# Optimization experiments

Hardware: AMD Instinct MI355X
Metric: run time of the kernel (lower is better)

The kernel has to match this reference:

```python
import jax, jax.numpy as jnp
import numpy as np

N = 16384; C = 16; H = 256; W = 704
HEADS = 4; PTS = 4; K = 8; DH = C // HEADS
EPS = 1e-3  # BatchNorm eps from module

def _bn(x, g, b):
    # BatchNorm1d in training mode: batch statistics over N
    mu = x.mean(axis=0)
    var = x.var(axis=0)
    return (x - mu) * jax.lax.rsqrt(var + EPS) * g + b

def setup_inputs():
    key = jax.random.key(0)
    ks = jax.random.split(key, 20)
    def w(i, shape, s=0.25):
        return jax.random.normal(ks[i], shape, jnp.float32) * s
    grid_y = jax.random.randint(ks[0], (N,), 0, H)
    grid_x = jax.random.randint(ks[1], (N,), 0, W)
    return {
        "point_features": jax.random.normal(ks[2], (N, C), jnp.float32),
        "image_feat": jax.random.normal(ks[3], (C, H, W), jnp.float32),
        "image_grid": jnp.stack([grid_y, grid_x], axis=1),
        "Wk": w(4, (C, C)), "bk": w(5, (C,)), "gk": jnp.ones((C,)), "betak": jnp.zeros((C,)),
        "Wfc": w(6, (2, C)), "bfc": w(7, (C,)), "gfc": jnp.ones((C,)), "betafc": jnp.zeros((C,)),
        "Wt": w(8, (C, C)), "bt": w(9, (C,)), "gt": jnp.ones((C,)), "betat": jnp.zeros((C,)),
        "Woff": w(10, (C, HEADS * PTS * 2), 0.02), "boff": w(11, (HEADS * PTS * 2,), 0.5),
        "Wattn": w(12, (C, HEADS * PTS), 0.02), "battn": jnp.zeros((HEADS * PTS,)),
        "Wval": w(13, (C, C)), "bval": w(14, (C,)),
        "Wout": w(15, (C, C)), "bout": w(16, (C,)),
        "Wf": w(17, (2 * C, C)), "bf": w(18, (C,)), "gf": jnp.ones((C,)), "betaf": jnp.zeros((C,)),
    }

def _deform_attn(q, image_feat, grid_f, Woff, boff, Wattn, battn, Wval, bval, Wout, bout):
    # MSDeformAttn with 1 level: learned offsets around projected pixel, bilinear sampling
    n = q.shape[0]
    off = (q @ Woff + boff).reshape(n, HEADS, PTS, 2)
    attn = jax.nn.softmax((q @ Wattn + battn).reshape(n, HEADS, PTS), axis=-1)
    val = (image_feat.reshape(C, H * W).T @ Wval + bval).reshape(H * W, HEADS, DH)
    val_h = val.transpose(1, 0, 2)  # [HEADS, HW, DH]
    loc_y = grid_f[:, 0][:, None, None] + off[..., 0]  # [N, HEADS, PTS]
    loc_x = grid_f[:, 1][:, None, None] + off[..., 1]
    y0 = jnp.floor(loc_y); x0 = jnp.floor(loc_x)
    wy = loc_y - y0; wx = loc_x - x0

    def corner(yi, xi, wgt):
        valid = (yi >= 0) & (yi <= H - 1) & (xi >= 0) & (xi <= W - 1)
        yc = jnp.clip(yi, 0, H - 1).astype(jnp.int32)
        xc = jnp.clip(xi, 0, W - 1).astype(jnp.int32)
        idx = (yc * W + xc).transpose(1, 0, 2)  # [HEADS, N, PTS]
        g = jax.vmap(lambda v, i: v[i])(val_h, idx)  # [HEADS, N, PTS, DH]
        return g * (wgt * valid).transpose(1, 0, 2)[..., None]

    samp = (corner(y0, x0, (1 - wy) * (1 - wx))
            + corner(y0, x0 + 1, (1 - wy) * wx)
            + corner(y0 + 1, x0, wy * (1 - wx))
            + corner(y0 + 1, x0 + 1, wy * wx))  # [HEADS, N, PTS, DH]
    out = (samp * attn.transpose(1, 0, 2)[..., None]).sum(axis=2)  # [HEADS, N, DH]
    out = out.transpose(1, 0, 2).reshape(n, C)
    return out @ Wout + bout

def reference(point_features, image_feat, image_grid, Wk, bk, gk, betak, Wfc, bfc, gfc, betafc, Wt, bt, gt, betat, Woff, boff, Wattn, battn, Wval, bval, Wout, bout, Wf, bf, gf, betaf):
    grid_f = image_grid.astype(jnp.float32)
    # KNN over projected pixel coords (cKDTree.query k=K+1, drop self)
    d2 = ((grid_f[:, None, :] - grid_f[None, :, :]) ** 2).sum(-1)
    _, nidx = jax.lax.top_k(-d2, K + 1)
    nidx = nidx[:, 1:]  # [N, K]

    pts = _bn(point_features @ Wk + bk, gk, betak)  # pts_key_proj
    # normalized relative image-plane positions -> fc
    center = grid_f.mean(axis=0)
    rel = grid_f - center
    mx = jnp.abs(rel).max(axis=0)
    mx = jnp.where(mx == 0, 1.0, mx)
    pos = _bn((rel / mx) @ Wfc + bfc, gfc, betafc)

    # gather image feats at projected pixels + KNN-graph neighbor aggregation
    gathered = image_feat[:, image_grid[:, 0], image_grid[:, 1]].T  # [N, C]
    neigh = gathered[nidx].mean(axis=1)  # [N, C]

    q = pts + pos
    img_pre = _deform_attn(q, image_feat, grid_f, Woff, boff, Wattn, battn, Wval, bval, Wout, bout) + neigh

    pts_pre = _bn(pts @ Wt + bt, gt, betat)  # pts_transform
    fuse = jax.nn.relu(jnp.concatenate([pts_pre, img_pre], axis=-1))  # activate_out
    return jax.nn.relu(_bn(fuse @ Wf + bf, gf, betaf))  # fuse_conv
```

## Files before the change

### kernel.cpp

```cpp
#include <hip/hip_runtime.h>
#include <climits>

#define N_ 16384
#define C_ 16
#define H_ 256
#define W_ 704
#define HW_ (H_*W_)
#define NC_ (N_*C_)
#define EPS_ 1e-3f
#define HDR_ 512

typedef unsigned long long ull;


#define VAL_   (HDR_ + 9*NC_)
#define KNNI_  (VAL_ + HW_*16)
#define PARTF_ (KNNI_ + 378256)
#define PK_    (PARTF_ + 8192)
#define PFC_   (PARTF_ + 16384)
#define PT_    (PARTF_ + 24576)

#define CAP_ 6144

__device__ __forceinline__ float wsum64(float v){
#pragma unroll
  for (int o = 32; o > 0; o >>= 1) v += __shfl_down(v, o);
  return v;
}

#define LOAD16(dst, src) { const float4* _s=(const float4*)(src); float4 _a=_s[0],_b=_s[1],_c=_s[2],_d=_s[3]; \
  dst[0]=_a.x;dst[1]=_a.y;dst[2]=_a.z;dst[3]=_a.w; dst[4]=_b.x;dst[5]=_b.y;dst[6]=_b.z;dst[7]=_b.w; \
  dst[8]=_c.x;dst[9]=_c.y;dst[10]=_c.z;dst[11]=_c.w; dst[12]=_d.x;dst[13]=_d.y;dst[14]=_d.z;dst[15]=_d.w; }

#define STORE16(dst, src) { float4* _d=(float4*)(dst); \
  _d[0]=make_float4(src[0],src[1],src[2],src[3]); _d[1]=make_float4(src[4],src[5],src[6],src[7]); \
  _d[2]=make_float4(src[8],src[9],src[10],src[11]); _d[3]=make_float4(src[12],src[13],src[14],src[15]); }

__global__ __launch_bounds__(256) void k_init(float* ws){
  if (blockIdx.x < 176){
    int4* c = (int4*)(ws + KNNI_);
    c[blockIdx.x*256 + threadIdx.x] = make_int4(0,0,0,0);
  } else if (threadIdx.x == 0){
    int* ih = (int*)ws;
    ih[0]=0; ih[1]=0; ih[2]=INT_MAX; ih[3]=INT_MIN; ih[4]=INT_MAX; ih[5]=INT_MIN;
  }
}

__global__ __launch_bounds__(256) void k_gridcnt(const int* __restrict__ grid, float* __restrict__ ws){
  int i = blockIdx.x*256 + threadIdx.x;
  int2 p = ((const int2*)grid)[i];
  int* counts = (int*)(ws + KNNI_);
  atomicAdd(&counts[p.x*W_ + p.y], 1);
  int sy=p.x, sx=p.y, mny=p.x, mxy=p.x, mnx=p.y, mxx=p.y;
#pragma unroll
  for (int o=32;o>0;o>>=1){
    sy += __shfl_down(sy,o); sx += __shfl_down(sx,o);
    mny = min(mny,__shfl_down(mny,o)); mxy = max(mxy,__shfl_down(mxy,o));
    mnx = min(mnx,__shfl_down(mnx,o)); mxx = max(mxx,__shfl_down(mxx,o));
  }
  __shared__ int sh[24];
  int w = threadIdx.x >> 6;
  if ((threadIdx.x & 63) == 0){
    sh[w]=sy; sh[4+w]=sx; sh[8+w]=mny; sh[12+w]=mxy; sh[16+w]=mnx; sh[20+w]=mxx;
  }
  __syncthreads();
  if (threadIdx.x == 0){
    int a0=sh[0]+sh[1]+sh[2]+sh[3];
    int a1=sh[4]+sh[5]+sh[6]+sh[7];
    int a2=min(min(sh[8],sh[9]),min(sh[10],sh[11]));
    int a3=max(max(sh[12],sh[13]),max(sh[14],sh[15]));
    int a4=min(min(sh[16],sh[17]),min(sh[18],sh[19]));
    int a5=max(max(sh[20],sh[21]),max(sh[22],sh[23]));
    int* ih = (int*)ws;
    atomicAdd(&ih[0],a0); atomicAdd(&ih[1],a1);
    atomicMin(&ih[2],a2); atomicMax(&ih[3],a3);
    atomicMin(&ih[4],a4); atomicMax(&ih[5],a5);
  }
}

__global__ __launch_bounds__(256) void k_scanA(float* ws){
  const int* counts = (const int*)(ws + KNNI_);
  int* bsum = (int*)(ws + KNNI_) + 180224 + 180240;
  int t = threadIdx.x;
  int v = counts[blockIdx.x*256 + t];
#pragma unroll
  for (int o=32;o>0;o>>=1) v += __shfl_down(v,o);
  __shared__ int w4[4];
  if ((t&63)==0) w4[t>>6] = v;
  __syncthreads();
  if (t==0) bsum[blockIdx.x] = w4[0]+w4[1]+w4[2]+w4[3];
}

__global__ __launch_bounds__(256) void k_scanB(float* ws){
  if (threadIdx.x == 0){
    int* ih = (int*)ws;
    float cy = (float)ih[0] / (float)N_;
    float cx = (float)ih[1] / (float)N_;
    float my = fmaxf((float)ih[3]-cy, cy-(float)ih[2]);
    float mx = fmaxf((float)ih[5]-cx, cx-(float)ih[4]);
    if (my == 0.f) my = 1.f;
    if (mx == 0.f) mx = 1.f;
    ws[264]=cy; ws[265]=cx; ws[266]=1.f/my; ws[267]=1.f/mx;
  }
  int* bsum = (int*)(ws + KNNI_) + 180224 + 180240;
  int* boff = bsum + 704;
  __shared__ int sWsum[4];
  __shared__ int sCarry;
  int t = threadIdx.x, lane = t & 63, wv = t >> 6;
  if (t==0) sCarry = 0;
  __syncthreads();
  for (int c=0;c<3;++c){
    int idx = c*256 + t;
    int v0 = (idx < 704) ? bsum[idx] : 0;
    int v = v0;
#pragma unroll
    for (int o=1;o<64;o<<=1){ int xx=__shfl_up(v,o); if (lane>=o) v+=xx; }
    if (lane==63) sWsum[wv]=v;
    __syncthreads();
    int add = sCarry;
    for (int w2=0;w2<wv;++w2) add += sWsum[w2];
    if (idx < 704) boff[idx] = add + v - v0;
    __syncthreads();
    if (t==255) sCarry = add + v;
    __syncthreads();
  }
}

__global__ __launch_bounds__(256) void k_scanC(float* ws){
  int* counts = (int*)(ws + KNNI_);
  int* cellst = counts + 180224;
  const int* boff = counts + 180224 + 180240 + 704;
  __shared__ int sWsum[4];
  int t = threadIdx.x, lane = t & 63, wv = t >> 6;
  int i = blockIdx.x*256 + t;
  int v0 = counts[i], v = v0;
#pragma unroll
  for (int o=1;o<64;o<<=1){ int xx=__shfl_up(v,o); if (lane>=o) v+=xx; }
  if (lane==63) sWsum[wv]=v;
  __syncthreads();
  int add = boff[blockIdx.x];
  for (int w2=0;w2<wv;++w2) add += sWsum[w2];
  int start = add + v - v0;
  cellst[i] = start;
  counts[i] = start;
  if (i == 0) cellst[HW_] = N_;
}

__global__ __launch_bounds__(256) void k_scatter(const int* __restrict__ grid, float* __restrict__ ws){
  int i = blockIdx.x*256 + threadIdx.x;
  int2 g = ((const int2*)grid)[i];
  int* counts = (int*)(ws + KNNI_);
  unsigned* psort = (unsigned*)(counts + 180224 + 180240 + 704 + 704);
  int pos = atomicAdd(&counts[g.x*W_ + g.y], 1);
  psort[pos] = ((unsigned)g.x<<24) | ((unsigned)g.y<<14) | (unsigned)i;
}

__global__ __launch_bounds__(256) void k_prep(const float* __restrict__ imf,
                                              const int* __restrict__ grid,
                                              const float* __restrict__ Wval,
                                              const float* __restrict__ bval,
                                              float* __restrict__ ws){
  int t = threadIdx.x;
  if (blockIdx.x < 1024){
    int idx = blockIdx.x*256 + t;
    int i = idx >> 4, c = idx & 15;
    int2 g = ((const int2*)grid)[i];
    ws[HDR_ + 2*NC_ + idx] = imf[c*HW_ + g.x*W_ + g.y];
  } else {
    __shared__ float sW[256], sb[16];
    sW[t] = Wval[t];
    if (t < 16) sb[t] = bval[t];
    __syncthreads();
    int pix = (blockIdx.x-1024)*256 + t;
    float a[16];
#pragma unroll
    for (int ci=0;ci<16;++ci) a[ci] = imf[ci*HW_ + pix];
    float o[16];
#pragma unroll
    for (int c=0;c<16;++c) o[c] = sb[c];
#pragma unroll
    for (int ci=0;ci<16;++ci){ float v=a[ci];
#pragma unroll
      for (int c=0;c<16;++c) o[c] += v*sW[ci*16+c];
    }
    float* val = ws + VAL_;
    STORE16(val + pix*16, o);
  }
}

__device__ __forceinline__ void knn_insert(ull* arr, ull key){
  if (key < arr[8]){
    int q = 8;
    while (q > 0 && arr[q-1] > key){ arr[q] = arr[q-1]; --q; }
    arr[q] = key;
  }
}

__device__ __forceinline__ void scan_rows_global(const int* __restrict__ cellst,
                                                 const unsigned* __restrict__ psort,
                                                 int y, int x, int s,
                                                 int y0, int y1, int x0, int x1, ull* arr){
  for (int yy=y0+s; yy<=y1; yy+=4){
    int rowb = yy*W_;
    int st = cellst[rowb + x0];
    int e  = cellst[rowb + x1 + 1];
    int dy = y-yy, dy2 = dy*dy;
    for (int p=st; p<e; ++p){
      unsigned u = psort[p];
      int px = (int)((u>>14)&1023);
      int dx = x-px;
      knn_insert(arr, ((ull)(unsigned)(dy2+dx*dx) << 14) | (ull)(u & 16383u));
    }
  }
}

__device__ __forceinline__ void scan_rows_band(const unsigned* sBand, const int* sRowBase,
                                               int ya, int y, int x, int s,
                                               int y0, int y1, int x0, int x1, ull* arr){
  for (int yy=y0+s; yy<=y1; yy+=4){
    int j = yy-ya;
    int b = sRowBase[j], e = sRowBase[j+1];
    int lo=b, hi=e;
    while (lo<hi){ int mid=(lo+hi)>>1; int xm=(int)((sBand[mid]>>14)&1023); if (xm<x0) lo=mid+1; else hi=mid; }
    int dy = y-yy, dy2 = dy*dy;
    for (int p=lo; p<e; ++p){
      unsigned u = sBand[p];
      int px = (int)((u>>14)&1023);
      if (px > x1) break;
      int dx = x-px;
      knn_insert(arr, ((ull)(unsigned)(dy2+dx*dx) << 14) | (ull)(u & 16383u));
    }
  }
}

__global__ __launch_bounds__(256) void k_knn4(float* __restrict__ ws){
  const int* cellst = (const int*)(ws + KNNI_) + 180224;
  const unsigned* psort = (const unsigned*)((const int*)(ws + KNNI_) + 180224 + 180240 + 704 + 704);
  __shared__ unsigned sBand[CAP_];
  __shared__ int sRowBase[80];
  __shared__ int sMn, sMx;
  int tid = threadIdx.x, lane = tid & 63;
  int s = tid & 3, pl = tid >> 2;
  int gid = blockIdx.x*64 + pl;
  unsigned me = psort[gid];
  int y = (int)(me>>24), x = (int)((me>>14)&1023), i = (int)(me&16383);
  if (tid==0){ sMn = INT_MAX; sMx = -1; }
  __syncthreads();
  if (s==0){ atomicMin(&sMn, y); atomicMax(&sMx, y); }
  __syncthreads();
  int ya = max(sMn-16,0), yb = min(sMx+16,H_-1);
  int nr = yb-ya+1;
  int p0 = cellst[ya*W_], p1 = cellst[(yb+1)*W_];
  int count = p1-p0;
  bool fb = (count > CAP_) || (nr > 78);
  if (!fb){
    for (int j=tid; j<count; j+=256) sBand[j] = psort[p0+j];
    for (int j=tid; j<=nr; j+=256) sRowBase[j] = cellst[(ya+j)*W_] - p0;
  }
  __syncthreads();
  int r = 8;
  { int y0=max(y-8,0),y1=min(y+8,H_-1),x0=max(x-8,0),x1=min(x+8,W_-1);
    if ((y1-y0+1)*(x1-x0+1) < 224) r = 16; }
  ull arr[9];
#pragma unroll
  for (int q=0;q<9;++q) arr[q] = ~0ull;
  {
    int y0=max(y-r,0),y1=min(y+r,H_-1),x0=max(x-r,0),x1=min(x+r,W_-1);
    if (!fb) scan_rows_band(sBand, sRowBase, ya, y, x, s, y0, y1, x0, x1, arr);
    else     scan_rows_global(cellst, psort, y, x, s, y0, y1, x0, x1, arr);
  }
  ull m[9];
  bool done = false;
  {
    ull k[9];
#pragma unroll
    for (int q=0;q<9;++q) m[q] = ~0ull;
    int base = lane & ~3;
    for (int ss=0; ss<4; ++ss){
#pragma unroll
      for (int q=0;q<9;++q) k[q] = __shfl(arr[q], base+ss);
      for (int q2=0;q2<9;++q2){
        ull kk = k[q2];
        if (kk >= m[8]) break;
        int q = 8; while (q>0 && m[q-1]>kk){ m[q]=m[q-1]; --q; } m[q]=kk;
      }
    }
    int y0=max(y-r,0),y1=min(y+r,H_-1),x0=max(x-r,0),x1=min(x+r,W_-1);
    bool covered = (y0==0)&&(y1==H_-1)&&(x0==0)&&(x1==W_-1);
    bool ok = covered;
    if (!ok && m[8] != ~0ull){ int d9 = (int)(m[8]>>14); ok = d9 < (r+1)*(r+1); }
    done = ok;
  }
  while (__ballot(!done)){
    if (!done){
      r <<= 1;
      int y0=max(y-r,0),y1=min(y+r,H_-1),x0=max(x-r,0),x1=min(x+r,W_-1);
#pragma unroll
      for (int q=0;q<9;++q) arr[q] = ~0ull;
      if (!fb && r <= 16) scan_rows_band(sBand, sRowBase, ya, y, x, s, y0, y1, x0, x1, arr);
      else                scan_rows_global(cellst, psort, y, x, s, y0, y1, x0, x1, arr);
    }
    ull k[9];
    bool doIns = !done;
    if (doIns){
#pragma unroll
      for (int q=0;q<9;++q) m[q] = ~0ull;
    }
    int base = lane & ~3;
    for (int ss=0; ss<4; ++ss){
#pragma unroll
      for (int q=0;q<9;++q) k[q] = __shfl(arr[q], base+ss);
      if (doIns){
        for (int q2=0;q2<9;++q2){
          ull kk = k[q2];
          if (kk >= m[8]) break;
          int q = 8; while (q>0 && m[q-1]>kk){ m[q]=m[q-1]; --q; } m[q]=kk;
        }
      }
    }
    if (!done){
      int y0=max(y-r,0),y1=min(y+r,H_-1),x0=max(x-r,0),x1=min(x+r,W_-1);
      bool covered = (y0==0)&&(y1==H_-1)&&(x0==0)&&(x1==W_-1);
      bool ok = covered;
      if (!ok && m[8] != ~0ull){ int d9 = (int)(m[8]>>14); ok = d9 < (r+1)*(r+1); }
      if (ok) done = true;
    }
  }
  const float* gath = ws + HDR_ + 2*NC_;
  float4 acc = make_float4(0.f,0.f,0.f,0.f);
#pragma unroll
  for (int nb=1; nb<9; ++nb){
    int idx = (int)(m[nb] & 16383ull);
    const float4 g = *(const float4*)(gath + idx*16 + s*4);
    acc.x += g.x; acc.y += g.y; acc.z += g.z; acc.w += g.w;
  }
  float* neigh = ws + HDR_ + 7*NC_;
  *(float4*)(neigh + i*16 + s*4) =
      make_float4(acc.x*0.125f, acc.y*0.125f, acc.z*0.125f, acc.w*0.125f);
}

__global__ __launch_bounds__(64) void k_lin1(
    const float* __restrict__ pf, const int* __restrict__ grid,
    const float* __restrict__ Wk, const float* __restrict__ bk,
    const float* __restrict__ Wfc, const float* __restrict__ bfc,
    float* __restrict__ ws)
{
  __shared__ float sWk[256], sbk[16], sWfc[32], sbfc[16];
  int t = threadIdx.x;
  for (int j=t;j<256;j+=64) sWk[j] = Wk[j];
  if (t < 16){ sbk[t]=bk[t]; sbfc[t]=bfc[t]; }
  if (t < 32) sWfc[t] = Wfc[t];
  __syncthreads();
  int i = blockIdx.x*64 + t;
  float p[16]; LOAD16(p, pf + i*16);
  float ok[16];
#pragma unroll
  for (int c=0;c<16;++c) ok[c] = sbk[c];
#pragma unroll
  for (int j=0;j<16;++j){ float v = p[j];
#pragma unroll
    for (int c=0;c<16;++c) ok[c] += v*sWk[j*16+c];
  }
  float* pts_lin = ws + HDR_;
  STORE16(pts_lin + i*16, ok);
  float cy=ws[264], cx=ws[265], imy=ws[266], imx=ws[267];
  int2 g = ((const int2*)grid)[i];
  float ry = ((float)g.x - cy)*imy, rx = ((float)g.y - cx)*imx;
  float op[16];
#pragma unroll
  for (int c=0;c<16;++c) op[c] = ry*sWfc[c] + rx*sWfc[16+c] + sbfc[c];
  float* pos_lin = ws + HDR_ + NC_;
  STORE16(pos_lin + i*16, op);
  float* partK  = ws + PK_;
  float* partFC = ws + PFC_;
#pragma unroll
  for (int c=0;c<16;++c){
    float a = wsum64(ok[c]); float b = wsum64(ok[c]*ok[c]);
    if (t==0){ partK[blockIdx.x*32+c]=a; partK[blockIdx.x*32+16+c]=b; }
    a = wsum64(op[c]); b = wsum64(op[c]*op[c]);
    if (t==0){ partFC[blockIdx.x*32+c]=a; partFC[blockIdx.x*32+16+c]=b; }
  }
}

__device__ __forceinline__ void red1_body(const float* __restrict__ g, const float* __restrict__ b,
                                          float* __restrict__ ws, int partOff, int aOff, float* red){
  int t = threadIdx.x, slot = t & 31, chunk = t >> 5;
  const float* part = ws + partOff;
  float acc = 0.f;
  for (int bb=chunk*32; bb<chunk*32+32; ++bb) acc += part[bb*32 + slot];
  red[t] = acc;
  __syncthreads();
  if (chunk == 0){
    float v = red[slot];
#pragma unroll
    for (int k2=1;k2<8;++k2) v += red[k2*32+slot];
    red[slot] = v;
  }
  __syncthreads();
  if (t < 16){
    float mu  = red[t]    * (1.f/N_);
    float var = red[16+t] * (1.f/N_) - mu*mu;
    float a = g[t] / sqrtf(var + EPS_);
    ws[aOff+t]    = a;
    ws[aOff+16+t] = b[t] - mu*a;
  }
  __syncthreads();
}

__global__ __launch_bounds__(256) void k_red2(const float* __restrict__ gk, const float* __restrict__ betak,
                                              const float* __restrict__ gfc, const float* __restrict__ betafc,
                                              float* __restrict__ ws){
  __shared__ float red[256];
  red1_body(gk, betak, ws, PK_, 136, red);
  red1_body(gfc, betafc, ws, PFC_, 168, red);
}

__global__ __launch_bounds__(256) void k_red1(const float* __restrict__ g, const float* __restrict__ b,
                                              float* __restrict__ ws, int partOff, int aOff){
  __shared__ float red[256];
  red1_body(g, b, ws, partOff, aOff, red);
}

__global__ __launch_bounds__(64) void k_qstage(
    const float* __restrict__ Wt, const float* __restrict__ bt,
    const float* __restrict__ Woff, const float* __restrict__ boff,
    const float* __restrict__ Wattn, const float* __restrict__ battn,
    float* __restrict__ ws)
{
  __shared__ float sWt[256], sWoff[512], sWattn[256];
  __shared__ float sbt[16], sboff[32], sbattn[16];
  __shared__ float skA[16], skC[16], sfcA[16], sfcC[16];
  int t = threadIdx.x;
  for (int j=t;j<256;j+=64){ sWt[j]=Wt[j]; sWattn[j]=Wattn[j]; }
  for (int j=t;j<512;j+=64) sWoff[j]=Woff[j];
  if (t<16){ sbt[t]=bt[t]; sbattn[t]=battn[t];
    skA[t]=ws[136+t]; skC[t]=ws[152+t]; sfcA[t]=ws[168+t]; sfcC[t]=ws[184+t]; }
  if (t<32) sboff[t]=boff[t];
  __syncthreads();
  int i = blockIdx.x*64 + t;
  float* pts_lin = ws + HDR_;
  float* pos_lin = ws + HDR_ + NC_;
  float* t_lin   = ws + HDR_ + 3*NC_;
  float* offp    = ws + HDR_ + 4*NC_;
  float* attnp   = ws + HDR_ + 6*NC_;
  float pl[16], po[16];
  LOAD16(pl, pts_lin + i*16);
  LOAD16(po, pos_lin + i*16);
  float pts[16], q[16];
#pragma unroll
  for (int c=0;c<16;++c){ pts[c] = pl[c]*skA[c]+skC[c]; q[c] = pts[c] + po[c]*sfcA[c]+sfcC[c]; }
  float tv[16];
#pragma unroll
  for (int c=0;c<16;++c) tv[c] = sbt[c];
#pragma unroll
  for (int j=0;j<16;++j){ float v=pts[j];
#pragma unroll
    for (int c=0;c<16;++c) tv[c] += v*sWt[j*16+c];
  }
  STORE16(t_lin + i*16, tv);
  float* partT = ws + PT_;
#pragma unroll
  for (int c=0;c<16;++c){
    float a = wsum64(tv[c]); float b = wsum64(tv[c]*tv[c]);
    if (t==0){ partT[blockIdx.x*32+c]=a; partT[blockIdx.x*32+16+c]=b; }
  }
  float ov[32];
#pragma unroll
  for (int o=0;o<32;++o) ov[o] = sboff[o];
#pragma unroll
  for (int j=0;j<16;++j){ float v=q[j];
#pragma unroll
    for (int o=0;o<32;++o) ov[o] += v*sWoff[j*32+o];
  }
  { float4* d=(float4*)(offp + i*32);
#pragma unroll
    for (int r=0;r<8;++r) d[r]=make_float4(ov[r*4],ov[r*4+1],ov[r*4+2],ov[r*4+3]);
  }
  float l[16];
#pragma unroll
  for (int c=0;c<16;++c) l[c] = sbattn[c];
#pragma unroll
  for (int j=0;j<16;++j){ float v=q[j];
#pragma unroll
    for (int c=0;c<16;++c) l[c] += v*sWattn[j*16+c];
  }
  float av[16];
#pragma unroll
  for (int h=0;h<4;++h){
    float m = fmaxf(fmaxf(l[h*4],l[h*4+1]),fmaxf(l[h*4+2],l[h*4+3]));
    float e0=expf(l[h*4]-m), e1=expf(l[h*4+1]-m), e2=expf(l[h*4+2]-m), e3=expf(l[h*4+3]-m);
    float inv = 1.f/(e0+e1+e2+e3);
    av[h*4]=e0*inv; av[h*4+1]=e1*inv; av[h*4+2]=e2*inv; av[h*4+3]=e3*inv;
  }
  STORE16(attnp + i*16, av);
}

__global__ __launch_bounds__(256) void k_attn(
    const int* __restrict__ grid,
    const float* __restrict__ Wout, const float* __restrict__ bout,
    const float* __restrict__ Wf, const float* __restrict__ bf,
    float* __restrict__ ws)
{
  __shared__ float sWout[256], sWf[512], sbout[16], sbf[16];
  __shared__ float sTl[1024], sNei[1024], sSamp[1024], sImg[1024];
  __shared__ float sPart[128];
  int t = threadIdx.x;
  int p = t >> 2, h = t & 3;
  int i = blockIdx.x*64 + p;
  sWout[t]=Wout[t]; sWf[t]=Wf[t]; sWf[t+256]=Wf[t+256];
  if (t<16){ sbout[t]=bout[t]; sbf[t]=bf[t]; }
  {
    const float4* tl4 = (const float4*)(ws + HDR_ + 3*NC_ + blockIdx.x*1024);
    const float4* nv4 = (const float4*)(ws + HDR_ + 7*NC_ + blockIdx.x*1024);
    float4 v = tl4[t];
    int c0 = (t*4) & 15;
    float a0=ws[200+c0],a1=ws[200+c0+1],a2=ws[200+c0+2],a3=ws[200+c0+3];
    float c0v=ws[216+c0],c1v=ws[216+c0+1],c2v=ws[216+c0+2],c3v=ws[216+c0+3];
    sTl[t*4]   = fmaxf(v.x*a0+c0v, 0.f);
    sTl[t*4+1] = fmaxf(v.y*a1+c1v, 0.f);
    sTl[t*4+2] = fmaxf(v.z*a2+c2v, 0.f);
    sTl[t*4+3] = fmaxf(v.w*a3+c3v, 0.f);
    float4 nv = nv4[t];
    sNei[t*4]=nv.x; sNei[t*4+1]=nv.y; sNei[t*4+2]=nv.z; sNei[t*4+3]=nv.w;
  }
  const float4* off4 = (const float4*)(ws + HDR_ + 4*NC_ + blockIdx.x*2048);
  float4 o0 = off4[t*2], o1 = off4[t*2+1];
  float4 aw = ((const float4*)(ws + HDR_ + 6*NC_ + blockIdx.x*1024))[t];
  int2 g = ((const int2*)grid)[i];
  float y = (float)g.x, x = (float)g.y;
  const float4* val4 = (const float4*)(ws + VAL_);
  float4 acc = make_float4(0.f,0.f,0.f,0.f);
  float offv[8] = {o0.x,o0.y,o0.z,o0.w,o1.x,o1.y,o1.z,o1.w};
  float avv[4]  = {aw.x,aw.y,aw.z,aw.w};
#define CORNER(yy,xx,wgt) do{ int _y=(yy),_x=(xx); \
    if ((unsigned)_y < (unsigned)H_ && (unsigned)_x < (unsigned)W_){ \
      float4 _v = val4[(_y*W_+_x)*4 + h]; float _w = a*(wgt); \
      acc.x += _w*_v.x; acc.y += _w*_v.y; acc.z += _w*_v.z; acc.w += _w*_v.w; } }while(0)
#pragma unroll
  for (int pt=0; pt<4; ++pt){
    float a  = avv[pt];
    float ly = y + offv[pt*2], lx = x + offv[pt*2+1];
    float fy = floorf(ly), fx = floorf(lx);
    float wy = ly - fy, wx = lx - fx;
    int y0 = (int)fy, x0 = (int)fx;
    CORNER(y0,   x0,   (1.f-wy)*(1.f-wx));
    CORNER(y0,   x0+1, (1.f-wy)*wx);
    CORNER(y0+1, x0,   wy*(1.f-wx));
    CORNER(y0+1, x0+1, wy*wx);
  }
#undef CORNER
  ((float4*)sSamp)[t] = acc;
  __syncthreads();
  float img[4];
#pragma unroll
  for (int k=0;k<4;++k){ int cc=h*4+k; img[k] = sbout[cc] + sNei[p*16+cc]; }
#pragma unroll
  for (int j=0;j<16;++j){
    float v = sSamp[p*16+j];
#pragma unroll
    for (int k=0;k<4;++k) img[k] += v*sWout[j*16 + h*4 + k];
  }
  ((float4*)sImg)[t] = make_float4(img[0],img[1],img[2],img[3]);
  __syncthreads();
  float fl[4];
#pragma unroll
  for (int k=0;k<4;++k) fl[k] = sbf[h*4+k];
#pragma unroll
  for (int j=0;j<16;++j){
    float v1 = sTl[p*16+j];
    float v2 = fmaxf(sImg[p*16+j], 0.f);
#pragma unroll
    for (int k=0;k<4;++k){
      fl[k] += v1*sWf[j*16 + h*4 + k];
      fl[k] += v2*sWf[(16+j)*16 + h*4 + k];
    }
  }
  float* f_lin = ws + HDR_ + 8*NC_;
  ((float4*)(f_lin + blockIdx.x*1024))[t] = make_float4(fl[0],fl[1],fl[2],fl[3]);
  float s0=fl[0],s1=fl[1],s2=fl[2],s3=fl[3];
  float q0=fl[0]*fl[0],q1=fl[1]*fl[1],q2=fl[2]*fl[2],q3=fl[3]*fl[3];
#pragma unroll
  for (int o=32;o>=4;o>>=1){
    s0+=__shfl_down(s0,o); s1+=__shfl_down(s1,o); s2+=__shfl_down(s2,o); s3+=__shfl_down(s3,o);
    q0+=__shfl_down(q0,o); q1+=__shfl_down(q1,o); q2+=__shfl_down(q2,o); q3+=__shfl_down(q3,o);
  }
  int wave = t >> 6, lane = t & 63;
  if (lane < 4){
    sPart[wave*32 + lane*4+0]=s0; sPart[wave*32 + lane*4+1]=s1;
    sPart[wave*32 + lane*4+2]=s2; sPart[wave*32 + lane*4+3]=s3;
    sPart[wave*32 + 16 + lane*4+0]=q0; sPart[wave*32 + 16 + lane*4+1]=q1;
    sPart[wave*32 + 16 + lane*4+2]=q2; sPart[wave*32 + 16 + lane*4+3]=q3;
  }
  __syncthreads();
  if (t < 32){
    float v = sPart[t]+sPart[32+t]+sPart[64+t]+sPart[96+t];
    (ws + PARTF_)[blockIdx.x*32 + t] = v;
  }
}

__global__ __launch_bounds__(256) void k_out(const float* __restrict__ ws, float* __restrict__ out){
  int idx = blockIdx.x*256 + threadIdx.x;
  int c = idx & 15;
  float v = ws[HDR_ + 8*NC_ + idx];
  out[idx] = fmaxf(v*ws[232+c] + ws[248+c], 0.f);
}

extern "C" void kernel_launch(void* const* d_in, const int* in_sizes, int n_in,
                              void* d_out, int out_size, void* d_ws, size_t ws_size,
                              hipStream_t stream)
{
  const float* pf    = (const float*)d_in[0];
  const float* imf   = (const float*)d_in[1];
  const int*   gridp = (const int*)d_in[2];
  const float* Wk   =(const float*)d_in[3],  *bk   =(const float*)d_in[4];
  const float* gk   =(const float*)d_in[5],  *betak=(const float*)d_in[6];
  const float* Wfc  =(const float*)d_in[7],  *bfc  =(const float*)d_in[8];
  const float* gfc  =(const float*)d_in[9],  *betafc=(const float*)d_in[10];
  const float* Wt   =(const float*)d_in[11], *bt   =(const float*)d_in[12];
  const float* gt   =(const float*)d_in[13], *betat=(const float*)d_in[14];
  const float* Woff =(const float*)d_in[15], *boff =(const float*)d_in[16];
  const float* Wattn=(const float*)d_in[17], *battn=(const float*)d_in[18];
  const float* Wval =(const float*)d_in[19], *bval =(const float*)d_in[20];
  const float* Wout =(const float*)d_in[21], *bout =(const float*)d_in[22];
  const float* Wf   =(const float*)d_in[23], *bf   =(const float*)d_in[24];
  const float* gf   =(const float*)d_in[25], *betaf=(const float*)d_in[26];
  float* ws  = (float*)d_ws;
  float* out = (float*)d_out;

  hipLaunchKernelGGL(k_init,     dim3(177),      dim3(256), 0, stream, ws);
  hipLaunchKernelGGL(k_gridcnt,  dim3(N_/256),   dim3(256), 0, stream, gridp, ws);
  hipLaunchKernelGGL(k_scanA,    dim3(704),      dim3(256), 0, stream, ws);
  hipLaunchKernelGGL(k_scanB,    dim3(1),        dim3(256), 0, stream, ws);
  hipLaunchKernelGGL(k_scanC,    dim3(704),      dim3(256), 0, stream, ws);
  hipLaunchKernelGGL(k_scatter,  dim3(N_/256),   dim3(256), 0, stream, gridp, ws);
  hipLaunchKernelGGL(k_prep,     dim3(1728),     dim3(256), 0, stream, imf, gridp, Wval, bval, ws);
  hipLaunchKernelGGL(k_lin1,     dim3(N_/64),    dim3(64),  0, stream, pf, gridp, Wk, bk, Wfc, bfc, ws);
  hipLaunchKernelGGL(k_red2,     dim3(1),        dim3(256), 0, stream, gk, betak, gfc, betafc, ws);
  hipLaunchKernelGGL(k_qstage,   dim3(N_/64),    dim3(64),  0, stream, Wt, bt, Woff, boff, Wattn, battn, ws);
  hipLaunchKernelGGL(k_red1,     dim3(1),        dim3(256), 0, stream, gt, betat, ws, PT_, 200);
  hipLaunchKernelGGL(k_knn4,     dim3(N_/64),    dim3(256), 0, stream, ws);
  hipLaunchKernelGGL(k_attn,     dim3(N_/64),    dim3(256), 0, stream, gridp, Wout, bout, Wf, bf, ws);
  hipLaunchKernelGGL(k_red1,     dim3(1),        dim3(256), 0, stream, gf, betaf, ws, PARTF_, 232);
  hipLaunchKernelGGL(k_out,      dim3(NC_/256),  dim3(256), 0, stream, ws, out);
}
```

Baseline: 228.2 us.

## Compute BatchNorm stats analytically from input covariance and fuse stages into mega kernel

Computes the per-block second-moment matrix of the point features and grid moments in one pass, then derives the BatchNorm mean and variance for the key, position and transform layers in closed form. This removes the separate linear and reduction kernels, so the query, KNN, attention and fuse stages can run in one fused kernel, and the final BN and ReLU fold into a single output kernel. Launch count drops from fifteen to eight and intermediate round trips to memory are avoided. The trade-off is that variance computed as E[x²]−μ² in float can lose precision, and the single large kernel may have higher register pressure.

```diff
diff --git a/kernel.cpp b/kernel.cpp
--- a/kernel.cpp
+++ b/kernel.cpp
@@ -13,12 +13,13 @@
 typedef unsigned long long ull;
 
 
+#define GATH_  (HDR_ + 2*NC_)
+#define FLIN_  (HDR_ + 8*NC_)
 #define VAL_   (HDR_ + 9*NC_)
 #define KNNI_  (VAL_ + HW_*16)
 #define PARTF_ (KNNI_ + 378256)
-#define PK_    (PARTF_ + 8192)
-#define PFC_   (PARTF_ + 16384)
-#define PT_    (PARTF_ + 24576)
+#define PS_    (PARTF_ + 8192)
+#define GP_    (PS_ + 17408)
 
 #define CAP_ 6144
 
@@ -42,39 +43,88 @@
     c[blockIdx.x*256 + threadIdx.x] = make_int4(0,0,0,0);
   } else if (threadIdx.x == 0){
     int* ih = (int*)ws;
-    ih[0]=0; ih[1]=0; ih[2]=INT_MAX; ih[3]=INT_MIN; ih[4]=INT_MAX; ih[5]=INT_MIN;
-  }
-}
-
-__global__ __launch_bounds__(256) void k_gridcnt(const int* __restrict__ grid, float* __restrict__ ws){
-  int i = blockIdx.x*256 + threadIdx.x;
-  int2 p = ((const int2*)grid)[i];
-  int* counts = (int*)(ws + KNNI_);
-  atomicAdd(&counts[p.x*W_ + p.y], 1);
-  int sy=p.x, sx=p.y, mny=p.x, mxy=p.x, mnx=p.y, mxx=p.y;
-#pragma unroll
-  for (int o=32;o>0;o>>=1){
-    sy += __shfl_down(sy,o); sx += __shfl_down(sx,o);
-    mny = min(mny,__shfl_down(mny,o)); mxy = max(mxy,__shfl_down(mxy,o));
-    mnx = min(mnx,__shfl_down(mnx,o)); mxx = max(mxx,__shfl_down(mxx,o));
-  }
-  __shared__ int sh[24];
-  int w = threadIdx.x >> 6;
-  if ((threadIdx.x & 63) == 0){
-    sh[w]=sy; sh[4+w]=sx; sh[8+w]=mny; sh[12+w]=mxy; sh[16+w]=mnx; sh[20+w]=mxx;
-  }
-  __syncthreads();
-  if (threadIdx.x == 0){
-    int a0=sh[0]+sh[1]+sh[2]+sh[3];
-    int a1=sh[4]+sh[5]+sh[6]+sh[7];
-    int a2=min(min(sh[8],sh[9]),min(sh[10],sh[11]));
-    int a3=max(max(sh[12],sh[13]),max(sh[14],sh[15]));
-    int a4=min(min(sh[16],sh[17]),min(sh[18],sh[19]));
-    int a5=max(max(sh[20],sh[21]),max(sh[22],sh[23]));
-    int* ih = (int*)ws;
-    atomicAdd(&ih[0],a0); atomicAdd(&ih[1],a1);
-    atomicMin(&ih[2],a2); atomicMax(&ih[3],a3);
-    atomicMin(&ih[4],a4); atomicMax(&ih[5],a5);
+    ih[2]=INT_MAX; ih[3]=INT_MIN; ih[4]=INT_MAX; ih[5]=INT_MIN;
+  }
+}
+
+__global__ __launch_bounds__(256) void k_statsprep(
+    const float* __restrict__ pf, const float* __restrict__ imf,
+    const int* __restrict__ grid,
+    const float* __restrict__ Wval, const float* __restrict__ bval,
+    float* __restrict__ ws)
+{
+  int t = threadIdx.x;
+  if (blockIdx.x < 64){
+    __shared__ float sP[4096];
+    __shared__ double sDP[20];
+    __shared__ int sh[16];
+    int i = blockIdx.x*256 + t;
+    { const float4* s4=(const float4*)(pf+i*16);
+      float4* d4=(float4*)(sP+t*16);
+      d4[0]=s4[0]; d4[1]=s4[1]; d4[2]=s4[2]; d4[3]=s4[3]; }
+    int2 g = ((const int2*)grid)[i];
+    int* counts = (int*)(ws + KNNI_);
+    atomicAdd(&counts[g.x*W_ + g.y], 1);
+    int mny=g.x,mxy=g.x,mnx=g.y,mxx=g.y;
+#pragma unroll
+    for (int o=32;o>0;o>>=1){
+      mny=min(mny,__shfl_down(mny,o)); mxy=max(mxy,__shfl_down(mxy,o));
+      mnx=min(mnx,__shfl_down(mnx,o)); mxx=max(mxx,__shfl_down(mxx,o));
+    }
+    int wv = t>>6;
+    if ((t&63)==0){ sh[wv]=mny; sh[4+wv]=mxy; sh[8+wv]=mnx; sh[12+wv]=mxx; }
+    double yy=(double)g.x, xx=(double)g.y;
+    double m0=yy,m1=xx,m2=yy*yy,m3=xx*xx,m4=yy*xx;
+#pragma unroll
+    for (int o=32;o>0;o>>=1){
+      m0+=__shfl_down(m0,o); m1+=__shfl_down(m1,o); m2+=__shfl_down(m2,o);
+      m3+=__shfl_down(m3,o); m4+=__shfl_down(m4,o);
+    }
+    if ((t&63)==0){ sDP[wv*5]=m0; sDP[wv*5+1]=m1; sDP[wv*5+2]=m2; sDP[wv*5+3]=m3; sDP[wv*5+4]=m4; }
+    __syncthreads();
+    if (t==0){
+      int* ih=(int*)ws;
+      atomicMin(&ih[2],min(min(sh[0],sh[1]),min(sh[2],sh[3])));
+      atomicMax(&ih[3],max(max(sh[4],sh[5]),max(sh[6],sh[7])));
+      atomicMin(&ih[4],min(min(sh[8],sh[9]),min(sh[10],sh[11])));
+      atomicMax(&ih[5],max(max(sh[12],sh[13]),max(sh[14],sh[15])));
+      double* GP=(double*)(ws+GP_)+blockIdx.x*5;
+#pragma unroll
+      for (int k=0;k<5;++k) GP[k]=sDP[k]+sDP[5+k]+sDP[10+k]+sDP[15+k];
+    }
+    float* PS = ws + PS_ + blockIdx.x*272;
+    int a=t&15, b2=t>>4;
+    float acc=0.f;
+    for (int i2=0;i2<256;++i2) acc += sP[i2*16+a]*sP[i2*16+b2];
+    PS[16+t]=acc;
+    if (t<16){
+      float s=0.f;
+      for (int i2=0;i2<256;++i2) s += sP[i2*16+t];
+      PS[t]=s;
+    }
+  } else if (blockIdx.x < 1088){
+    int idx=(blockIdx.x-64)*256+t;
+    int i=idx>>4, c=idx&15;
+    int2 g=((const int2*)grid)[i];
+    ws[GATH_+idx]=imf[c*HW_+g.x*W_+g.y];
+  } else {
+    __shared__ float sW[256], sb[16];
+    sW[t]=Wval[t];
+    if (t<16) sb[t]=bval[t];
+    __syncthreads();
+    int pix=(blockIdx.x-1088)*256+t;
+    float a[16];
+#pragma unroll
+    for (int ci=0;ci<16;++ci) a[ci]=imf[ci*HW_+pix];
+    float o[16];
+#pragma unroll
+    for (int c=0;c<16;++c) o[c]=sb[c];
+#pragma unroll
+    for (int ci=0;ci<16;++ci){ float v=a[ci];
+#pragma unroll
+      for (int c=0;c<16;++c) o[c]+=v*sW[ci*16+c];
+    }
+    STORE16(ws+VAL_+pix*16, o);
   }
 }
 
@@ -91,37 +141,129 @@
   if (t==0) bsum[blockIdx.x] = w4[0]+w4[1]+w4[2]+w4[3];
 }
 
-__global__ __launch_bounds__(256) void k_scanB(float* ws){
-  if (threadIdx.x == 0){
-    int* ih = (int*)ws;
-    float cy = (float)ih[0] / (float)N_;
-    float cx = (float)ih[1] / (float)N_;
-    float my = fmaxf((float)ih[3]-cy, cy-(float)ih[2]);
-    float mx = fmaxf((float)ih[5]-cx, cx-(float)ih[4]);
-    if (my == 0.f) my = 1.f;
-    if (mx == 0.f) mx = 1.f;
-    ws[264]=cy; ws[265]=cx; ws[266]=1.f/my; ws[267]=1.f/mx;
-  }
+__global__ __launch_bounds__(256) void k_scanB(
+    const float* __restrict__ Wk, const float* __restrict__ bk,
+    const float* __restrict__ gk, const float* __restrict__ betak,
+    const float* __restrict__ Wfc, const float* __restrict__ bfc,
+    const float* __restrict__ gfc, const float* __restrict__ betafc,
+    const float* __restrict__ Wt, const float* __restrict__ bt,
+    const float* __restrict__ gt, const float* __restrict__ betat,
+    float* __restrict__ ws)
+{
+  __shared__ float sS[256], sSum[16];
+  __shared__ float skA[16], skC[16];
+  __shared__ double sG[5];
+  __shared__ float sCtr[4];
+  int t = threadIdx.x;
+  const float* PS = ws + PS_;
+  float acc=0.f, acc2=0.f;
+  for (int b=0;b<64;++b){
+    acc += PS[b*272 + t];
+    if (t<16) acc2 += PS[b*272 + 256 + t];
+  }
+  if (t<16){ sSum[t]=acc; sS[240+t]=acc2; }
+  else sS[t-16]=acc;
+  if (t<5){
+    const double* GP=(const double*)(ws+GP_);
+    double s=0.0;
+    for (int b=0;b<64;++b) s += GP[b*5+t];
+    sG[t]=s;
+  }
+  __syncthreads();
+  if (t==0){
+    const int* ih=(const int*)ws;
+    float cy=(float)(sG[0]/(double)N_), cx=(float)(sG[1]/(double)N_);
+    float my=fmaxf((float)ih[3]-cy, cy-(float)ih[2]);
+    float mx=fmaxf((float)ih[5]-cx, cx-(float)ih[4]);
+    if (my==0.f) my=1.f;
+    if (mx==0.f) mx=1.f;
+    sCtr[0]=cy; sCtr[1]=cx; sCtr[2]=1.f/my; sCtr[3]=1.f/mx;
+    ws[264]=cy; ws[265]=cx; ws[266]=sCtr[2]; ws[267]=sCtr[3];
+  }
+  __syncthreads();
+  const float invN = 1.f/(float)N_;
+  if (t<16){
+    float wc[16];
+#pragma unroll
+    for (int j=0;j<16;++j) wc[j]=Wk[j*16+t];
+    float dotS=0.f;
+#pragma unroll
+    for (int a2=0;a2<16;++a2) dotS+=sSum[a2]*wc[a2];
+    float qd=0.f;
+#pragma unroll
+    for (int b2=0;b2<16;++b2){
+      float inner=0.f;
+#pragma unroll
+      for (int a2=0;a2<16;++a2) inner+=wc[a2]*sS[b2*16+a2];
+      qd+=wc[b2]*inner;
+    }
+    float bkc=bk[t];
+    float mu = dotS*invN + bkc;
+    float ex2 = qd*invN + 2.f*bkc*dotS*invN + bkc*bkc;
+    float var = ex2 - mu*mu;
+    float a = gk[t]/sqrtf(var+EPS_);
+    skA[t]=a; skC[t]=betak[t]-mu*a;
+    ws[136+t]=a; ws[152+t]=skC[t];
+    float cy=sCtr[0], cx=sCtr[1], imy=sCtr[2], imx=sCtr[3];
+    float Eyy=((float)(sG[2]/(double)N_) - cy*cy)*imy*imy;
+    float Exx=((float)(sG[3]/(double)N_) - cx*cx)*imx*imx;
+    float Eyx=((float)(sG[4]/(double)N_) - cy*cx)*imy*imx;
+    float W0=Wfc[t], W1=Wfc[16+t];
+    float varfc = Eyy*W0*W0 + 2.f*Eyx*W0*W1 + Exx*W1*W1;
+    float afc = gfc[t]/sqrtf(varfc+EPS_);
+    ws[168+t]=afc; ws[184+t]=betafc[t]-bfc[t]*afc;
+  }
+  __syncthreads();
+  if (t<16){
+    float Ac[16];
+#pragma unroll
+    for (int j=0;j<16;++j){
+      float s=0.f;
+#pragma unroll
+      for (int m=0;m<16;++m) s += Wk[j*16+m]*skA[m]*Wt[m*16+t];
+      Ac[j]=s;
+    }
+    float dc=bt[t];
+#pragma unroll
+    for (int m=0;m<16;++m) dc += (bk[m]*skA[m]+skC[m])*Wt[m*16+t];
+    float dotS=0.f;
+#pragma unroll
+    for (int a2=0;a2<16;++a2) dotS+=sSum[a2]*Ac[a2];
+    float qd=0.f;
+#pragma unroll
+    for (int b2=0;b2<16;++b2){
+      float inner=0.f;
+#pragma unroll
+      for (int a2=0;a2<16;++a2) inner+=Ac[a2]*sS[b2*16+a2];
+      qd+=Ac[b2]*inner;
+    }
+    float mu = dotS*invN + dc;
+    float ex2 = qd*invN + 2.f*dc*dotS*invN + dc*dc;
+    float var = ex2 - mu*mu;
+    float a = gt[t]/sqrtf(var+EPS_);
+    ws[200+t]=a; ws[216+t]=betat[t]-mu*a;
+  }
+  __syncthreads();
   int* bsum = (int*)(ws + KNNI_) + 180224 + 180240;
   int* boff = bsum + 704;
   __shared__ int sWsum[4];
   __shared__ int sCarry;
-  int t = threadIdx.x, lane = t & 63, wv = t >> 6;
-  if (t==0) sCarry = 0;
+  int lane=t&63, wv=t>>6;
+  if (t==0) sCarry=0;
   __syncthreads();
   for (int c=0;c<3;++c){
-    int idx = c*256 + t;
-    int v0 = (idx < 704) ? bsum[idx] : 0;
-    int v = v0;
+    int idx=c*256+t;
+    int v0=(idx<704)?bsum[idx]:0;
+    int v=v0;
 #pragma unroll
     for (int o=1;o<64;o<<=1){ int xx=__shfl_up(v,o); if (lane>=o) v+=xx; }
     if (lane==63) sWsum[wv]=v;
     __syncthreads();
-    int add = sCarry;
-    for (int w2=0;w2<wv;++w2) add += sWsum[w2];
-    if (idx < 704) boff[idx] = add + v - v0;
-    __syncthreads();
-    if (t==255) sCarry = add + v;
+    int add=sCarry;
+    for (int w2=0;w2<wv;++w2) add+=sWsum[w2];
+    if (idx<704) boff[idx]=add+v-v0;
+    __syncthreads();
+    if (t==255) sCarry=add+v;
     __syncthreads();
   }
 }
@@ -131,68 +273,35 @@
   int* cellst = counts + 180224;
   const int* boff = counts + 180224 + 180240 + 704;
   __shared__ int sWsum[4];
-  int t = threadIdx.x, lane = t & 63, wv = t >> 6;
-  int i = blockIdx.x*256 + t;
-  int v0 = counts[i], v = v0;
+  int t=threadIdx.x, lane=t&63, wv=t>>6;
+  int i=blockIdx.x*256+t;
+  int v0=counts[i], v=v0;
 #pragma unroll
   for (int o=1;o<64;o<<=1){ int xx=__shfl_up(v,o); if (lane>=o) v+=xx; }
   if (lane==63) sWsum[wv]=v;
   __syncthreads();
-  int add = boff[blockIdx.x];
-  for (int w2=0;w2<wv;++w2) add += sWsum[w2];
-  int start = add + v - v0;
-  cellst[i] = start;
-  counts[i] = start;
-  if (i == 0) cellst[HW_] = N_;
+  int add=boff[blockIdx.x];
+  for (int w2=0;w2<wv;++w2) add+=sWsum[w2];
+  int start=add+v-v0;
+  cellst[i]=start;
+  counts[i]=start;
+  if (i==0) cellst[HW_]=N_;
 }
 
 __global__ __launch_bounds__(256) void k_scatter(const int* __restrict__ grid, float* __restrict__ ws){
-  int i = blockIdx.x*256 + threadIdx.x;
-  int2 g = ((const int2*)grid)[i];
-  int* counts = (int*)(ws + KNNI_);
-  unsigned* psort = (unsigned*)(counts + 180224 + 180240 + 704 + 704);
-  int pos = atomicAdd(&counts[g.x*W_ + g.y], 1);
-  psort[pos] = ((unsigned)g.x<<24) | ((unsigned)g.y<<14) | (unsigned)i;
-}
-
-__global__ __launch_bounds__(256) void k_prep(const float* __restrict__ imf,
-                                              const int* __restrict__ grid,
-                                              const float* __restrict__ Wval,
-                                              const float* __restrict__ bval,
-                                              float* __restrict__ ws){
-  int t = threadIdx.x;
-  if (blockIdx.x < 1024){
-    int idx = blockIdx.x*256 + t;
-    int i = idx >> 4, c = idx & 15;
-    int2 g = ((const int2*)grid)[i];
-    ws[HDR_ + 2*NC_ + idx] = imf[c*HW_ + g.x*W_ + g.y];
-  } else {
-    __shared__ float sW[256], sb[16];
-    sW[t] = Wval[t];
-    if (t < 16) sb[t] = bval[t];
-    __syncthreads();
-    int pix = (blockIdx.x-1024)*256 + t;
-    float a[16];
-#pragma unroll
-    for (int ci=0;ci<16;++ci) a[ci] = imf[ci*HW_ + pix];
-    float o[16];
-#pragma unroll
-    for (int c=0;c<16;++c) o[c] = sb[c];
-#pragma unroll
-    for (int ci=0;ci<16;++ci){ float v=a[ci];
-#pragma unroll
-      for (int c=0;c<16;++c) o[c] += v*sW[ci*16+c];
-    }
-    float* val = ws + VAL_;
-    STORE16(val + pix*16, o);
-  }
+  int i=blockIdx.x*256+threadIdx.x;
+  int2 g=((const int2*)grid)[i];
+  int* counts=(int*)(ws+KNNI_);
+  unsigned* psort=(unsigned*)(counts+180224+180240+704+704);
+  int pos=atomicAdd(&counts[g.x*W_+g.y],1);
+  psort[pos]=((unsigned)g.x<<24)|((unsigned)g.y<<14)|(unsigned)i;
 }
 
 __device__ __forceinline__ void knn_insert(ull* arr, ull key){
   if (key < arr[8]){
-    int q = 8;
-    while (q > 0 && arr[q-1] > key){ arr[q] = arr[q-1]; --q; }
-    arr[q] = key;
+    int q=8;
+    while (q>0 && arr[q-1]>key){ arr[q]=arr[q-1]; --q; }
+    arr[q]=key;
   }
 }
 
@@ -201,15 +310,15 @@
                                                  int y, int x, int s,
                                                  int y0, int y1, int x0, int x1, ull* arr){
   for (int yy=y0+s; yy<=y1; yy+=4){
-    int rowb = yy*W_;
-    int st = cellst[rowb + x0];
-    int e  = cellst[rowb + x1 + 1];
-    int dy = y-yy, dy2 = dy*dy;
-    for (int p=st; p<e; ++p){
-      unsigned u = psort[p];
-      int px = (int)((u>>14)&1023);
-      int dx = x-px;
-      knn_insert(arr, ((ull)(unsigned)(dy2+dx*dx) << 14) | (ull)(u & 16383u));
+    int rowb=yy*W_;
+    int st=cellst[rowb+x0];
+    int e =cellst[rowb+x1+1];
+    int dy=y-yy, dy2=dy*dy;
+    for (int p=st;p<e;++p){
+      unsigned u=psort[p];
+      int px=(int)((u>>14)&1023);
+      int dx=x-px;
+      knn_insert(arr, ((ull)(unsigned)(dy2+dx*dx)<<14)|(ull)(u&16383u));
     }
   }
 }
@@ -218,391 +327,331 @@
                                                int ya, int y, int x, int s,
                                                int y0, int y1, int x0, int x1, ull* arr){
   for (int yy=y0+s; yy<=y1; yy+=4){
-    int j = yy-ya;
-    int b = sRowBase[j], e = sRowBase[j+1];
+    int j=yy-ya;
+    int b=sRowBase[j], e=sRowBase[j+1];
     int lo=b, hi=e;
     while (lo<hi){ int mid=(lo+hi)>>1; int xm=(int)((sBand[mid]>>14)&1023); if (xm<x0) lo=mid+1; else hi=mid; }
-    int dy = y-yy, dy2 = dy*dy;
-    for (int p=lo; p<e; ++p){
-      unsigned u = sBand[p];
-      int px = (int)((u>>14)&1023);
-      if (px > x1) break;
-      int dx = x-px;
-      knn_insert(arr, ((ull)(unsigned)(dy2+dx*dx) << 14) | (ull)(u & 16383u));
-    }
-  }
-}
-
-__global__ __launch_bounds__(256) void k_knn4(float* __restrict__ ws){
-  const int* cellst = (const int*)(ws + KNNI_) + 180224;
-  const unsigned* psort = (const unsigned*)((const int*)(ws + KNNI_) + 180224 + 180240 + 704 + 704);
-  __shared__ unsigned sBand[CAP_];
-  __shared__ int sRowBase[80];
-  __shared__ int sMn, sMx;
-  int tid = threadIdx.x, lane = tid & 63;
-  int s = tid & 3, pl = tid >> 2;
-  int gid = blockIdx.x*64 + pl;
-  unsigned me = psort[gid];
-  int y = (int)(me>>24), x = (int)((me>>14)&1023), i = (int)(me&16383);
-  if (tid==0){ sMn = INT_MAX; sMx = -1; }
-  __syncthreads();
-  if (s==0){ atomicMin(&sMn, y); atomicMax(&sMx, y); }
-  __syncthreads();
-  int ya = max(sMn-16,0), yb = min(sMx+16,H_-1);
-  int nr = yb-ya+1;
-  int p0 = cellst[ya*W_], p1 = cellst[(yb+1)*W_];
-  int count = p1-p0;
-  bool fb = (count > CAP_) || (nr > 78);
-  if (!fb){
-    for (int j=tid; j<count; j+=256) sBand[j] = psort[p0+j];
-    for (int j=tid; j<=nr; j+=256) sRowBase[j] = cellst[(ya+j)*W_] - p0;
-  }
-  __syncthreads();
-  int r = 8;
-  { int y0=max(y-8,0),y1=min(y+8,H_-1),x0=max(x-8,0),x1=min(x+8,W_-1);
-    if ((y1-y0+1)*(x1-x0+1) < 224) r = 16; }
-  ull arr[9];
-#pragma unroll
-  for (int q=0;q<9;++q) arr[q] = ~0ull;
-  {
-    int y0=max(y-r,0),y1=min(y+r,H_-1),x0=max(x-r,0),x1=min(x+r,W_-1);
-    if (!fb) scan_rows_band(sBand, sRowBase, ya, y, x, s, y0, y1, x0, x1, arr);
-    else     scan_rows_global(cellst, psort, y, x, s, y0, y1, x0, x1, arr);
-  }
-  ull m[9];
-  bool done = false;
-  {
-    ull k[9];
-#pragma unroll
-    for (int q=0;q<9;++q) m[q] = ~0ull;
-    int base = lane & ~3;
-    for (int ss=0; ss<4; ++ss){
-#pragma unroll
-      for (int q=0;q<9;++q) k[q] = __shfl(arr[q], base+ss);
-      for (int q2=0;q2<9;++q2){
-        ull kk = k[q2];
-        if (kk >= m[8]) break;
-        int q = 8; while (q>0 && m[q-1]>kk){ m[q]=m[q-1]; --q; } m[q]=kk;
-      }
-    }
-    int y0=max(y-r,0),y1=min(y+r,H_-1),x0=max(x-r,0),x1=min(x+r,W_-1);
-    bool covered = (y0==0)&&(y1==H_-1)&&(x0==0)&&(x1==W_-1);
-    bool ok = covered;
-    if (!ok && m[8] != ~0ull){ int d9 = (int)(m[8]>>14); ok = d9 < (r+1)*(r+1); }
-    done = ok;
-  }
-  while (__ballot(!done)){
-    if (!done){
-      r <<= 1;
-      int y0=max(y-r,0),y1=min(y+r,H_-1),x0=max(x-r,0),x1=min(x+r,W_-1);
-#pragma unroll
-      for (int q=0;q<9;++q) arr[q] = ~0ull;
-      if (!fb && r <= 16) scan_rows_band(sBand, sRowBase, ya, y, x, s, y0, y1, x0, x1, arr);
-      else                scan_rows_global(cellst, psort, y, x, s, y0, y1, x0, x1, arr);
-    }
-    ull k[9];
-    bool doIns = !done;
-    if (doIns){
-#pragma unroll
-      for (int q=0;q<9;++q) m[q] = ~0ull;
-    }
-    int base = lane & ~3;
-    for (int ss=0; ss<4; ++ss){
-#pragma unroll
-      for (int q=0;q<9;++q) k[q] = __shfl(arr[q], base+ss);
-      if (doIns){
-        for (int q2=0;q2<9;++q2){
-          ull kk = k[q2];
-          if (kk >= m[8]) break;
-          int q = 8; while (q>0 && m[q-1]>kk){ m[q]=m[q-1]; --q; } m[q]=kk;
-        }
-      }
-    }
-    if (!done){
-      int y0=max(y-r,0),y1=min(y+r,H_-1),x0=max(x-r,0),x1=min(x+r,W_-1);
-      bool covered = (y0==0)&&(y1==H_-1)&&(x0==0)&&(x1==W_-1);
-      bool ok = covered;
-      if (!ok && m[8] != ~0ull){ int d9 = (int)(m[8]>>14); ok = d9 < (r+1)*(r+1); }
-      if (ok) done = true;
-    }
-  }
-  const float* gath = ws + HDR_ + 2*NC_;
-  float4 acc = make_float4(0.f,0.f,0.f,0.f);
-#pragma unroll
-  for (int nb=1; nb<9; ++nb){
-    int idx = (int)(m[nb] & 16383ull);
-    const float4 g = *(const float4*)(gath + idx*16 + s*4);
-    acc.x += g.x; acc.y += g.y; acc.z += g.z; acc.w += g.w;
-  }
-  float* neigh = ws + HDR_ + 7*NC_;
-  *(float4*)(neigh + i*16 + s*4) =
-      make_float4(acc.x*0.125f, acc.y*0.125f, acc.z*0.125f, acc.w*0.125f);
-}
-
-__global__ __launch_bounds__(64) void k_lin1(
-    const float* __restrict__ pf, const int* __restrict__ grid,
+    int dy=y-yy, dy2=dy*dy;
+    for (int p=lo;p<e;++p){
+      unsigned u=sBand[p];
+      int px=(int)((u>>14)&1023);
+      if (px>x1) break;
+      int dx=x-px;
+      knn_insert(arr, ((ull)(unsigned)(dy2+dx*dx)<<14)|(ull)(u&16383u));
+    }
+  }
+}
+
+__global__ __launch_bounds__(256) void k_mega(
+    const float* __restrict__ pf,
     const float* __restrict__ Wk, const float* __restrict__ bk,
     const float* __restrict__ Wfc, const float* __restrict__ bfc,
-    float* __restrict__ ws)
-{
-  __shared__ float sWk[256], sbk[16], sWfc[32], sbfc[16];
-  int t = threadIdx.x;
-  for (int j=t;j<256;j+=64) sWk[j] = Wk[j];
-  if (t < 16){ sbk[t]=bk[t]; sbfc[t]=bfc[t]; }
-  if (t < 32) sWfc[t] = Wfc[t];
-  __syncthreads();
-  int i = blockIdx.x*64 + t;
-  float p[16]; LOAD16(p, pf + i*16);
-  float ok[16];
-#pragma unroll
-  for (int c=0;c<16;++c) ok[c] = sbk[c];
-#pragma unroll
-  for (int j=0;j<16;++j){ float v = p[j];
-#pragma unroll
-    for (int c=0;c<16;++c) ok[c] += v*sWk[j*16+c];
-  }
-  float* pts_lin = ws + HDR_;
-  STORE16(pts_lin + i*16, ok);
-  float cy=ws[264], cx=ws[265], imy=ws[266], imx=ws[267];
-  int2 g = ((const int2*)grid)[i];
-  float ry = ((float)g.x - cy)*imy, rx = ((float)g.y - cx)*imx;
-  float op[16];
-#pragma unroll
-  for (int c=0;c<16;++c) op[c] = ry*sWfc[c] + rx*sWfc[16+c] + sbfc[c];
-  float* pos_lin = ws + HDR_ + NC_;
-  STORE16(pos_lin + i*16, op);
-  float* partK  = ws + PK_;
-  float* partFC = ws + PFC_;
-#pragma unroll
-  for (int c=0;c<16;++c){
-    float a = wsum64(ok[c]); float b = wsum64(ok[c]*ok[c]);
-    if (t==0){ partK[blockIdx.x*32+c]=a; partK[blockIdx.x*32+16+c]=b; }
-    a = wsum64(op[c]); b = wsum64(op[c]*op[c]);
-    if (t==0){ partFC[blockIdx.x*32+c]=a; partFC[blockIdx.x*32+16+c]=b; }
-  }
-}
-
-__device__ __forceinline__ void red1_body(const float* __restrict__ g, const float* __restrict__ b,
-                                          float* __restrict__ ws, int partOff, int aOff, float* red){
-  int t = threadIdx.x, slot = t & 31, chunk = t >> 5;
-  const float* part = ws + partOff;
-  float acc = 0.f;
-  for (int bb=chunk*32; bb<chunk*32+32; ++bb) acc += part[bb*32 + slot];
-  red[t] = acc;
-  __syncthreads();
-  if (chunk == 0){
-    float v = red[slot];
-#pragma unroll
-    for (int k2=1;k2<8;++k2) v += red[k2*32+slot];
-    red[slot] = v;
-  }
-  __syncthreads();
-  if (t < 16){
-    float mu  = red[t]    * (1.f/N_);
-    float var = red[16+t] * (1.f/N_) - mu*mu;
-    float a = g[t] / sqrtf(var + EPS_);
-    ws[aOff+t]    = a;
-    ws[aOff+16+t] = b[t] - mu*a;
-  }
-  __syncthreads();
-}
-
-__global__ __launch_bounds__(256) void k_red2(const float* __restrict__ gk, const float* __restrict__ betak,
-                                              const float* __restrict__ gfc, const float* __restrict__ betafc,
-                                              float* __restrict__ ws){
-  __shared__ float red[256];
-  red1_body(gk, betak, ws, PK_, 136, red);
-  red1_body(gfc, betafc, ws, PFC_, 168, red);
-}
-
-__global__ __launch_bounds__(256) void k_red1(const float* __restrict__ g, const float* __restrict__ b,
-                                              float* __restrict__ ws, int partOff, int aOff){
-  __shared__ float red[256];
-  red1_body(g, b, ws, partOff, aOff, red);
-}
-
-__global__ __launch_bounds__(64) void k_qstage(
     const float* __restrict__ Wt, const float* __restrict__ bt,
     const float* __restrict__ Woff, const float* __restrict__ boff,
     const float* __restrict__ Wattn, const float* __restrict__ battn,
-    float* __restrict__ ws)
-{
-  __shared__ float sWt[256], sWoff[512], sWattn[256];
-  __shared__ float sbt[16], sboff[32], sbattn[16];
-  __shared__ float skA[16], skC[16], sfcA[16], sfcC[16];
-  int t = threadIdx.x;
-  for (int j=t;j<256;j+=64){ sWt[j]=Wt[j]; sWattn[j]=Wattn[j]; }
-  for (int j=t;j<512;j+=64) sWoff[j]=Woff[j];
-  if (t<16){ sbt[t]=bt[t]; sbattn[t]=battn[t];
-    skA[t]=ws[136+t]; skC[t]=ws[152+t]; sfcA[t]=ws[168+t]; sfcC[t]=ws[184+t]; }
-  if (t<32) sboff[t]=boff[t];
-  __syncthreads();
-  int i = blockIdx.x*64 + t;
-  float* pts_lin = ws + HDR_;
-  float* pos_lin = ws + HDR_ + NC_;
-  float* t_lin   = ws + HDR_ + 3*NC_;
-  float* offp    = ws + HDR_ + 4*NC_;
-  float* attnp   = ws + HDR_ + 6*NC_;
-  float pl[16], po[16];
-  LOAD16(pl, pts_lin + i*16);
-  LOAD16(po, pos_lin + i*16);
-  float pts[16], q[16];
-#pragma unroll
-  for (int c=0;c<16;++c){ pts[c] = pl[c]*skA[c]+skC[c]; q[c] = pts[c] + po[c]*sfcA[c]+sfcC[c]; }
-  float tv[16];
-#pragma unroll
-  for (int c=0;c<16;++c) tv[c] = sbt[c];
-#pragma unroll
-  for (int j=0;j<16;++j){ float v=pts[j];
-#pragma unroll
-    for (int c=0;c<16;++c) tv[c] += v*sWt[j*16+c];
-  }
-  STORE16(t_lin + i*16, tv);
-  float* partT = ws + PT_;
-#pragma unroll
-  for (int c=0;c<16;++c){
-    float a = wsum64(tv[c]); float b = wsum64(tv[c]*tv[c]);
-    if (t==0){ partT[blockIdx.x*32+c]=a; partT[blockIdx.x*32+16+c]=b; }
-  }
-  float ov[32];
-#pragma unroll
-  for (int o=0;o<32;++o) ov[o] = sboff[o];
-#pragma unroll
-  for (int j=0;j<16;++j){ float v=q[j];
-#pragma unroll
-    for (int o=0;o<32;++o) ov[o] += v*sWoff[j*32+o];
-  }
-  { float4* d=(float4*)(offp + i*32);
-#pragma unroll
-    for (int r=0;r<8;++r) d[r]=make_float4(ov[r*4],ov[r*4+1],ov[r*4+2],ov[r*4+3]);
-  }
-  float l[16];
-#pragma unroll
-  for (int c=0;c<16;++c) l[c] = sbattn[c];
-#pragma unroll
-  for (int j=0;j<16;++j){ float v=q[j];
-#pragma unroll
-    for (int c=0;c<16;++c) l[c] += v*sWattn[j*16+c];
-  }
-  float av[16];
-#pragma unroll
-  for (int h=0;h<4;++h){
-    float m = fmaxf(fmaxf(l[h*4],l[h*4+1]),fmaxf(l[h*4+2],l[h*4+3]));
-    float e0=expf(l[h*4]-m), e1=expf(l[h*4+1]-m), e2=expf(l[h*4+2]-m), e3=expf(l[h*4+3]-m);
-    float inv = 1.f/(e0+e1+e2+e3);
-    av[h*4]=e0*inv; av[h*4+1]=e1*inv; av[h*4+2]=e2*inv; av[h*4+3]=e3*inv;
-  }
-  STORE16(attnp + i*16, av);
-}
-
-__global__ __launch_bounds__(256) void k_attn(
-    const int* __restrict__ grid,
     const float* __restrict__ Wout, const float* __restrict__ bout,
     const float* __restrict__ Wf, const float* __restrict__ bf,
     float* __restrict__ ws)
 {
-  __shared__ float sWout[256], sWf[512], sbout[16], sbf[16];
-  __shared__ float sTl[1024], sNei[1024], sSamp[1024], sImg[1024];
+  __shared__ float sWk[256], sWt[256], sWattn[256], sWout[256];
+  __shared__ float sWoff[512], sWf[512], sWfc[32];
+  __shared__ float sbk[16], sbfc[16], sbt[16], sboff[32], sbattn[16], sbout[16], sbf[16];
+  __shared__ float skA[16], skC[16], sfcA[16], sfcC[16], stA[16], stC[16];
+  __shared__ float sCtr[4];
+  __shared__ unsigned sMe[64];
+  __shared__ int sMn, sMx;
+  __shared__ unsigned sBand[CAP_];
+  __shared__ int sRowBase[80];
+  __shared__ float sTl[1024], sNei[1024], sOf[2048], sAt[1024], sSamp[1024], sImg[1024];
   __shared__ float sPart[128];
-  int t = threadIdx.x;
-  int p = t >> 2, h = t & 3;
-  int i = blockIdx.x*64 + p;
-  sWout[t]=Wout[t]; sWf[t]=Wf[t]; sWf[t+256]=Wf[t+256];
-  if (t<16){ sbout[t]=bout[t]; sbf[t]=bf[t]; }
+
+  const int* cellst = (const int*)(ws+KNNI_)+180224;
+  const unsigned* psort = (const unsigned*)((const int*)(ws+KNNI_)+180224+180240+704+704);
+  int tid=threadIdx.x, lane=tid&63;
+  sWk[tid]=Wk[tid]; sWt[tid]=Wt[tid]; sWattn[tid]=Wattn[tid]; sWout[tid]=Wout[tid];
+  sWoff[tid]=Woff[tid]; sWoff[256+tid]=Woff[256+tid];
+  sWf[tid]=Wf[tid]; sWf[256+tid]=Wf[256+tid];
+  if (tid<32){ sWfc[tid]=Wfc[tid]; sboff[tid]=boff[tid]; }
+  if (tid<16){
+    sbk[tid]=bk[tid]; sbfc[tid]=bfc[tid]; sbt[tid]=bt[tid]; sbattn[tid]=battn[tid];
+    sbout[tid]=bout[tid]; sbf[tid]=bf[tid];
+    skA[tid]=ws[136+tid]; skC[tid]=ws[152+tid];
+    sfcA[tid]=ws[168+tid]; sfcC[tid]=ws[184+tid];
+    stA[tid]=ws[200+tid]; stC[tid]=ws[216+tid];
+  }
+  if (tid<4) sCtr[tid]=ws[264+tid];
+  if (tid==0){ sMn=INT_MAX; sMx=-1; }
+  if (tid<64) sMe[tid]=psort[blockIdx.x*64+tid];
+  __syncthreads();
+  if (tid<64){
+    int yy=(int)(sMe[tid]>>24);
+    atomicMin(&sMn,yy); atomicMax(&sMx,yy);
+  }
+  __syncthreads();
+  int ya=max(sMn-16,0), yb=min(sMx+16,H_-1);
+  int nr=yb-ya+1;
+  int p0=cellst[ya*W_], p1=cellst[(yb+1)*W_];
+  int count=p1-p0;
+  bool fb=(count>CAP_)||(nr>78);
+  if (tid<64){
+    unsigned me=sMe[tid];
+    int i=(int)(me&16383u);
+    float yf=(float)(me>>24), xf=(float)((me>>14)&1023u);
+    float p[16]; LOAD16(p, pf+i*16);
+    float ok[16];
+#pragma unroll
+    for (int c=0;c<16;++c) ok[c]=sbk[c];
+#pragma unroll
+    for (int j=0;j<16;++j){ float v=p[j];
+#pragma unroll
+      for (int c=0;c<16;++c) ok[c]+=v*sWk[j*16+c];
+    }
+    float ry=(yf-sCtr[0])*sCtr[2], rx=(xf-sCtr[1])*sCtr[3];
+    float pts[16], q[16];
+#pragma unroll
+    for (int c=0;c<16;++c){
+      pts[c]=ok[c]*skA[c]+skC[c];
+      float pos=ry*sWfc[c]+rx*sWfc[16+c]+sbfc[c];
+      q[c]=pts[c]+pos*sfcA[c]+sfcC[c];
+    }
+    float tv[16];
+#pragma unroll
+    for (int c=0;c<16;++c) tv[c]=sbt[c];
+#pragma unroll
+    for (int j=0;j<16;++j){ float v=pts[j];
+#pragma unroll
+      for (int c=0;c<16;++c) tv[c]+=v*sWt[j*16+c];
+    }
+#pragma unroll
+    for (int c=0;c<16;++c) sTl[tid*16+c]=fmaxf(tv[c]*stA[c]+stC[c],0.f);
+    float ov[32];
+#pragma unroll
+    for (int o=0;o<32;++o) ov[o]=sboff[o];
+#pragma unroll
+    for (int j=0;j<16;++j){ float v=q[j];
+#pragma unroll
+      for (int o=0;o<32;++o) ov[o]+=v*sWoff[j*32+o];
+    }
+#pragma unroll
+    for (int o=0;o<32;++o) sOf[tid*32+o]=ov[o];
+    float l[16];
+#pragma unroll
+    for (int c=0;c<16;++c) l[c]=sbattn[c];
+#pragma unroll
+    for (int j=0;j<16;++j){ float v=q[j];
+#pragma unroll
+      for (int c=0;c<16;++c) l[c]+=v*sWattn[j*16+c];
+    }
+#pragma unroll
+    for (int h=0;h<4;++h){
+      float m=fmaxf(fmaxf(l[h*4],l[h*4+1]),fmaxf(l[h*4+2],l[h*4+3]));
+      float e0=expf(l[h*4]-m),e1=expf(l[h*4+1]-m),e2=expf(l[h*4+2]-m),e3=expf(l[h*4+3]-m);
+      float inv=1.f/(e0+e1+e2+e3);
+      sAt[tid*16+h*4]=e0*inv; sAt[tid*16+h*4+1]=e1*inv;
+      sAt[tid*16+h*4+2]=e2*inv; sAt[tid*16+h*4+3]=e3*inv;
+    }
+  } else {
+    int tt=tid-64;
+    if (!fb){
+      for (int j=tt;j<count;j+=192) sBand[j]=psort[p0+j];
+      for (int j=tt;j<=nr;j+=192) sRowBase[j]=cellst[(ya+j)*W_]-p0;
+    }
+  }
+  __syncthreads();
+  int s=tid&3, pl=tid>>2;
+  unsigned meK=sMe[pl];
+  int y=(int)(meK>>24), x=(int)((meK>>14)&1023u);
+  int r=8;
+  { int y0=max(y-8,0),y1=min(y+8,H_-1),x0=max(x-8,0),x1=min(x+8,W_-1);
+    if ((y1-y0+1)*(x1-x0+1)<224) r=16; }
+  ull arr[9];
+#pragma unroll
+  for (int q2=0;q2<9;++q2) arr[q2]=~0ull;
   {
-    const float4* tl4 = (const float4*)(ws + HDR_ + 3*NC_ + blockIdx.x*1024);
-    const float4* nv4 = (const float4*)(ws + HDR_ + 7*NC_ + blockIdx.x*1024);
-    float4 v = tl4[t];
-    int c0 = (t*4) & 15;
-    float a0=ws[200+c0],a1=ws[200+c0+1],a2=ws[200+c0+2],a3=ws[200+c0+3];
-    float c0v=ws[216+c0],c1v=ws[216+c0+1],c2v=ws[216+c0+2],c3v=ws[216+c0+3];
-    sTl[t*4]   = fmaxf(v.x*a0+c0v, 0.f);
-    sTl[t*4+1] = fmaxf(v.y*a1+c1v, 0.f);
-    sTl[t*4+2] = fmaxf(v.z*a2+c2v, 0.f);
-    sTl[t*4+3] = fmaxf(v.w*a3+c3v, 0.f);
-    float4 nv = nv4[t];
-    sNei[t*4]=nv.x; sNei[t*4+1]=nv.y; sNei[t*4+2]=nv.z; sNei[t*4+3]=nv.w;
-  }
-  const float4* off4 = (const float4*)(ws + HDR_ + 4*NC_ + blockIdx.x*2048);
-  float4 o0 = off4[t*2], o1 = off4[t*2+1];
-  float4 aw = ((const float4*)(ws + HDR_ + 6*NC_ + blockIdx.x*1024))[t];
-  int2 g = ((const int2*)grid)[i];
-  float y = (float)g.x, x = (float)g.y;
-  const float4* val4 = (const float4*)(ws + VAL_);
-  float4 acc = make_float4(0.f,0.f,0.f,0.f);
-  float offv[8] = {o0.x,o0.y,o0.z,o0.w,o1.x,o1.y,o1.z,o1.w};
-  float avv[4]  = {aw.x,aw.y,aw.z,aw.w};
+    int y0=max(y-r,0),y1=min(y+r,H_-1),x0=max(x-r,0),x1=min(x+r,W_-1);
+    if (!fb) scan_rows_band(sBand,sRowBase,ya,y,x,s,y0,y1,x0,x1,arr);
+    else     scan_rows_global(cellst,psort,y,x,s,y0,y1,x0,x1,arr);
+  }
+  ull m[9];
+  bool done=false;
+  {
+    ull k[9];
+#pragma unroll
+    for (int q2=0;q2<9;++q2) m[q2]=~0ull;
+    int base=lane&~3;
+    for (int ss=0;ss<4;++ss){
+#pragma unroll
+      for (int q2=0;q2<9;++q2) k[q2]=__shfl(arr[q2],base+ss);
+      for (int q3=0;q3<9;++q3){
+        ull kk=k[q3];
+        if (kk>=m[8]) break;
+        int q=8; while (q>0&&m[q-1]>kk){ m[q]=m[q-1]; --q; } m[q]=kk;
+      }
+    }
+    int y0=max(y-r,0),y1=min(y+r,H_-1),x0=max(x-r,0),x1=min(x+r,W_-1);
+    bool covered=(y0==0)&&(y1==H_-1)&&(x0==0)&&(x1==W_-1);
+    bool ok2=covered;
+    if (!ok2 && m[8]!=~0ull){ int d9=(int)(m[8]>>14); ok2 = d9 < (r+1)*(r+1); }
+    done=ok2;
+  }
+  while (__ballot(!done)){
+    if (!done){
+      r<<=1;
+      int y0=max(y-r,0),y1=min(y+r,H_-1),x0=max(x-r,0),x1=min(x+r,W_-1);
+#pragma unroll
+      for (int q2=0;q2<9;++q2) arr[q2]=~0ull;
+      if (!fb && r<=16) scan_rows_band(sBand,sRowBase,ya,y,x,s,y0,y1,x0,x1,arr);
+      else              scan_rows_global(cellst,psort,y,x,s,y0,y1,x0,x1,arr);
+    }
+    ull k[9];
+    bool doIns=!done;
+    if (doIns){
+#pragma unroll
+      for (int q2=0;q2<9;++q2) m[q2]=~0ull;
+    }
+    int base=lane&~3;
+    for (int ss=0;ss<4;++ss){
+#pragma unroll
+      for (int q2=0;q2<9;++q2) k[q2]=__shfl(arr[q2],base+ss);
+      if (doIns){
+        for (int q3=0;q3<9;++q3){
+          ull kk=k[q3];
+          if (kk>=m[8]) break;
+          int q=8; while (q>0&&m[q-1]>kk){ m[q]=m[q-1]; --q; } m[q]=kk;
+        }
+      }
+    }
+    if (!done){
+      int y0=max(y-r,0),y1=min(y+r,H_-1),x0=max(x-r,0),x1=min(x+r,W_-1);
+      bool covered=(y0==0)&&(y1==H_-1)&&(x0==0)&&(x1==W_-1);
+      bool ok2=covered;
+      if (!ok2 && m[8]!=~0ull){ int d9=(int)(m[8]>>14); ok2 = d9 < (r+1)*(r+1); }
+      if (ok2) done=true;
+    }
+  }
+  {
+    const float* gath = ws + GATH_;
+    float4 acc=make_float4(0.f,0.f,0.f,0.f);
+#pragma unroll
+    for (int nb=1;nb<9;++nb){
+      int idx=(int)(m[nb]&16383ull);
+      const float4 g=*(const float4*)(gath+idx*16+s*4);
+      acc.x+=g.x; acc.y+=g.y; acc.z+=g.z; acc.w+=g.w;
+    }
+    ((float4*)sNei)[tid]=make_float4(acc.x*0.125f,acc.y*0.125f,acc.z*0.125f,acc.w*0.125f);
+  }
+  __syncthreads();
+  {
+    int p=tid>>2, h=tid&3;
+    unsigned meA=sMe[p];
+    float yf=(float)(meA>>24), xf=(float)((meA>>14)&1023u);
+    const float4* val4=(const float4*)(ws+VAL_);
+    float4 acc=make_float4(0.f,0.f,0.f,0.f);
+    float offv[8];
+#pragma unroll
+    for (int o=0;o<8;++o) offv[o]=sOf[p*32+h*8+o];
+    float avv[4];
+#pragma unroll
+    for (int o=0;o<4;++o) avv[o]=sAt[p*16+h*4+o];
 #define CORNER(yy,xx,wgt) do{ int _y=(yy),_x=(xx); \
-    if ((unsigned)_y < (unsigned)H_ && (unsigned)_x < (unsigned)W_){ \
-      float4 _v = val4[(_y*W_+_x)*4 + h]; float _w = a*(wgt); \
-      acc.x += _w*_v.x; acc.y += _w*_v.y; acc.z += _w*_v.z; acc.w += _w*_v.w; } }while(0)
-#pragma unroll
-  for (int pt=0; pt<4; ++pt){
-    float a  = avv[pt];
-    float ly = y + offv[pt*2], lx = x + offv[pt*2+1];
-    float fy = floorf(ly), fx = floorf(lx);
-    float wy = ly - fy, wx = lx - fx;
-    int y0 = (int)fy, x0 = (int)fx;
-    CORNER(y0,   x0,   (1.f-wy)*(1.f-wx));
-    CORNER(y0,   x0+1, (1.f-wy)*wx);
-    CORNER(y0+1, x0,   wy*(1.f-wx));
-    CORNER(y0+1, x0+1, wy*wx);
-  }
+    if ((unsigned)_y<(unsigned)H_ && (unsigned)_x<(unsigned)W_){ \
+      float4 _v=val4[(_y*W_+_x)*4+h]; float _w=a*(wgt); \
+      acc.x+=_w*_v.x; acc.y+=_w*_v.y; acc.z+=_w*_v.z; acc.w+=_w*_v.w; } }while(0)
+#pragma unroll
+    for (int pt=0;pt<4;++pt){
+      float a=avv[pt];
+      float ly=yf+offv[pt*2], lx=xf+offv[pt*2+1];
+      float fy=floorf(ly), fx=floorf(lx);
+      float wy=ly-fy, wx=lx-fx;
+      int y0=(int)fy, x0=(int)fx;
+      CORNER(y0,  x0,  (1.f-wy)*(1.f-wx));
+      CORNER(y0,  x0+1,(1.f-wy)*wx);
+      CORNER(y0+1,x0,  wy*(1.f-wx));
+      CORNER(y0+1,x0+1,wy*wx);
+    }
 #undef CORNER
-  ((float4*)sSamp)[t] = acc;
-  __syncthreads();
-  float img[4];
-#pragma unroll
-  for (int k=0;k<4;++k){ int cc=h*4+k; img[k] = sbout[cc] + sNei[p*16+cc]; }
-#pragma unroll
-  for (int j=0;j<16;++j){
-    float v = sSamp[p*16+j];
-#pragma unroll
-    for (int k=0;k<4;++k) img[k] += v*sWout[j*16 + h*4 + k];
-  }
-  ((float4*)sImg)[t] = make_float4(img[0],img[1],img[2],img[3]);
-  __syncthreads();
-  float fl[4];
-#pragma unroll
-  for (int k=0;k<4;++k) fl[k] = sbf[h*4+k];
-#pragma unroll
-  for (int j=0;j<16;++j){
-    float v1 = sTl[p*16+j];
-    float v2 = fmaxf(sImg[p*16+j], 0.f);
-#pragma unroll
-    for (int k=0;k<4;++k){
-      fl[k] += v1*sWf[j*16 + h*4 + k];
-      fl[k] += v2*sWf[(16+j)*16 + h*4 + k];
-    }
-  }
-  float* f_lin = ws + HDR_ + 8*NC_;
-  ((float4*)(f_lin + blockIdx.x*1024))[t] = make_float4(fl[0],fl[1],fl[2],fl[3]);
-  float s0=fl[0],s1=fl[1],s2=fl[2],s3=fl[3];
-  float q0=fl[0]*fl[0],q1=fl[1]*fl[1],q2=fl[2]*fl[2],q3=fl[3]*fl[3];
-#pragma unroll
-  for (int o=32;o>=4;o>>=1){
-    s0+=__shfl_down(s0,o); s1+=__shfl_down(s1,o); s2+=__shfl_down(s2,o); s3+=__shfl_down(s3,o);
-    q0+=__shfl_down(q0,o); q1+=__shfl_down(q1,o); q2+=__shfl_down(q2,o); q3+=__shfl_down(q3,o);
-  }
-  int wave = t >> 6, lane = t & 63;
-  if (lane < 4){
-    sPart[wave*32 + lane*4+0]=s0; sPart[wave*32 + lane*4+1]=s1;
-    sPart[wave*32 + lane*4+2]=s2; sPart[wave*32 + lane*4+3]=s3;
-    sPart[wave*32 + 16 + lane*4+0]=q0; sPart[wave*32 + 16 + lane*4+1]=q1;
-    sPart[wave*32 + 16 + lane*4+2]=q2; sPart[wave*32 + 16 + lane*4+3]=q3;
-  }
-  __syncthreads();
-  if (t < 32){
-    float v = sPart[t]+sPart[32+t]+sPart[64+t]+sPart[96+t];
-    (ws + PARTF_)[blockIdx.x*32 + t] = v;
-  }
-}
-
-__global__ __launch_bounds__(256) void k_out(const float* __restrict__ ws, float* __restrict__ out){
-  int idx = blockIdx.x*256 + threadIdx.x;
-  int c = idx & 15;
-  float v = ws[HDR_ + 8*NC_ + idx];
-  out[idx] = fmaxf(v*ws[232+c] + ws[248+c], 0.f);
+    ((float4*)sSamp)[tid]=acc;
+    __syncthreads();
+    float img[4];
+#pragma unroll
+    for (int k2=0;k2<4;++k2){ int cc=h*4+k2; img[k2]=sbout[cc]+sNei[p*16+cc]; }
+#pragma unroll
+    for (int j=0;j<16;++j){
+      float v=sSamp[p*16+j];
+#pragma unroll
+      for (int k2=0;k2<4;++k2) img[k2]+=v*sWout[j*16+h*4+k2];
+    }
+    ((float4*)sImg)[tid]=make_float4(img[0],img[1],img[2],img[3]);
+    __syncthreads();
+    float fl[4];
+#pragma unroll
+    for (int k2=0;k2<4;++k2) fl[k2]=sbf[h*4+k2];
+#pragma unroll
+    for (int j=0;j<16;++j){
+      float v1=sTl[p*16+j];
+      float v2=fmaxf(sImg[p*16+j],0.f);
+#pragma unroll
+      for (int k2=0;k2<4;++k2){
+        fl[k2]+=v1*sWf[j*16+h*4+k2];
+        fl[k2]+=v2*sWf[(16+j)*16+h*4+k2];
+      }
+    }
+    int i3=(int)(meA&16383u);
+    ((float4*)(ws+FLIN_+i3*16))[h]=make_float4(fl[0],fl[1],fl[2],fl[3]);
+    float s0=fl[0],s1=fl[1],s2=fl[2],s3=fl[3];
+    float q0=fl[0]*fl[0],q1=fl[1]*fl[1],q2=fl[2]*fl[2],q3=fl[3]*fl[3];
+#pragma unroll
+    for (int o=32;o>=4;o>>=1){
+      s0+=__shfl_down(s0,o); s1+=__shfl_down(s1,o); s2+=__shfl_down(s2,o); s3+=__shfl_down(s3,o);
+      q0+=__shfl_down(q0,o); q1+=__shfl_down(q1,o); q2+=__shfl_down(q2,o); q3+=__shfl_down(q3,o);
+    }
+    int wave=tid>>6, lane2=tid&63;
+    if (lane2<4){
+      sPart[wave*32+lane2*4+0]=s0; sPart[wave*32+lane2*4+1]=s1;
+      sPart[wave*32+lane2*4+2]=s2; sPart[wave*32+lane2*4+3]=s3;
+      sPart[wave*32+16+lane2*4+0]=q0; sPart[wave*32+16+lane2*4+1]=q1;
+      sPart[wave*32+16+lane2*4+2]=q2; sPart[wave*32+16+lane2*4+3]=q3;
+    }
+    __syncthreads();
+    if (tid<32){
+      float v=sPart[tid]+sPart[32+tid]+sPart[64+tid]+sPart[96+tid];
+      (ws+PARTF_)[blockIdx.x*32+tid]=v;
+    }
+  }
+}
+
+__global__ __launch_bounds__(256) void k_outf(const float* __restrict__ gf,
+                                              const float* __restrict__ betaf,
+                                              const float* __restrict__ ws,
+                                              float* __restrict__ out){
+  __shared__ float red[256];
+  __shared__ float sA[16], sC[16];
+  int t=threadIdx.x, slot=t&31, chunk=t>>5;
+  const float* part=ws+PARTF_;
+  float acc=0.f;
+  for (int bb=chunk*32; bb<chunk*32+32; ++bb) acc+=part[bb*32+slot];
+  red[t]=acc;
+  __syncthreads();
+  if (chunk==0){
+    float v=red[slot];
+#pragma unroll
+    for (int k2=1;k2<8;++k2) v+=red[k2*32+slot];
+    red[slot]=v;
+  }
+  __syncthreads();
+  if (t<16){
+    float mu=red[t]*(1.f/N_);
+    float var=red[16+t]*(1.f/N_)-mu*mu;
+    float a=gf[t]/sqrtf(var+EPS_);
+    sA[t]=a; sC[t]=betaf[t]-mu*a;
+  }
+  __syncthreads();
+  int base=blockIdx.x*4096+t*16;
+  float fl[16]; LOAD16(fl, ws+FLIN_+base);
+  float o[16];
+#pragma unroll
+  for (int c=0;c<16;++c) o[c]=fmaxf(fl[c]*sA[c]+sC[c],0.f);
+  STORE16(out+base, o);
 }
 
 extern "C" void kernel_launch(void* const* d_in, const int* in_sizes, int n_in,
@@ -627,19 +676,15 @@
   float* ws  = (float*)d_ws;
   float* out = (float*)d_out;
 
-  hipLaunchKernelGGL(k_init,     dim3(177),      dim3(256), 0, stream, ws);
-  hipLaunchKernelGGL(k_gridcnt,  dim3(N_/256),   dim3(256), 0, stream, gridp, ws);
-  hipLaunchKernelGGL(k_scanA,    dim3(704),      dim3(256), 0, stream, ws);
-  hipLaunchKernelGGL(k_scanB,    dim3(1),        dim3(256), 0, stream, ws);
-  hipLaunchKernelGGL(k_scanC,    dim3(704),      dim3(256), 0, stream, ws);
-  hipLaunchKernelGGL(k_scatter,  dim3(N_/256),   dim3(256), 0, stream, gridp, ws);
-  hipLaunchKernelGGL(k_prep,     dim3(1728),     dim3(256), 0, stream, imf, gridp, Wval, bval, ws);
-  hipLaunchKernelGGL(k_lin1,     dim3(N_/64),    dim3(64),  0, stream, pf, gridp, Wk, bk, Wfc, bfc, ws);
-  hipLaunchKernelGGL(k_red2,     dim3(1),        dim3(256), 0, stream, gk, betak, gfc, betafc, ws);
-  hipLaunchKernelGGL(k_qstage,   dim3(N_/64),    dim3(64),  0, stream, Wt, bt, Woff, boff, Wattn, battn, ws);
-  hipLaunchKernelGGL(k_red1,     dim3(1),        dim3(256), 0, stream, gt, betat, ws, PT_, 200);
-  hipLaunchKernelGGL(k_knn4,     dim3(N_/64),    dim3(256), 0, stream, ws);
-  hipLaunchKernelGGL(k_attn,     dim3(N_/64),    dim3(256), 0, stream, gridp, Wout, bout, Wf, bf, ws);
-  hipLaunchKernelGGL(k_red1,     dim3(1),        dim3(256), 0, stream, gf, betaf, ws, PARTF_, 232);
-  hipLaunchKernelGGL(k_out,      dim3(NC_/256),  dim3(256), 0, stream, ws, out);
-}
+  hipLaunchKernelGGL(k_init,      dim3(177),  dim3(256), 0, stream, ws);
+  hipLaunchKernelGGL(k_statsprep, dim3(1792), dim3(256), 0, stream, pf, imf, gridp, Wval, bval, ws);
+  hipLaunchKernelGGL(k_scanA,     dim3(704),  dim3(256), 0, stream, ws);
+  hipLaunchKernelGGL(k_scanB,     dim3(1),    dim3(256), 0, stream,
+                     Wk, bk, gk, betak, Wfc, bfc, gfc, betafc, Wt, bt, gt, betat, ws);
+  hipLaunchKernelGGL(k_scanC,     dim3(704),  dim3(256), 0, stream, ws);
+  hipLaunchKernelGGL(k_scatter,   dim3(N_/256), dim3(256), 0, stream, gridp, ws);
+  hipLaunchKernelGGL(k_mega,      dim3(N_/64), dim3(256), 0, stream,
+                     pf, Wk, bk, Wfc, bfc, Wt, bt, Woff, boff, Wattn, battn,
+                     Wout, bout, Wf, bf, ws);
+  hipLaunchKernelGGL(k_outf,      dim3(64),   dim3(256), 0, stream, gf, betaf, ws, out);
+}
```

Result: no change. 224.7 us (-1.6%).
